# Kernel optimization log

Measured on AMD Instinct MI355X. Metric: run time of the kernel, lower is better.

## Reference

```python
import jax, jax.numpy as jnp
import numpy as np

L = 8          # fixed number of instance labels (0 = background), all assumed present
DV = 0.5       # delta_v
DD = 1.5       # delta_d
LOSS_WEIGHT = 1.0


def _safe_norm(x, axis):
    sq = jnp.sum(x * x, axis=axis)
    pos = sq > 0
    return jnp.sqrt(jnp.where(pos, sq, 1.0)) * pos.astype(x.dtype)


def _per_image(emb, inst, kern, tmask):
    # emb: [D,H,W], inst: [H,W] int, kern/tmask: [H,W] float
    D, H, W = emb.shape
    HW = H * W
    tm = (tmask > 0.5).astype(inst.dtype)
    kb = (kern > 0.5).astype(inst.dtype)
    inst = inst * tm
    inst_k = (inst * kb).reshape(-1)          # kernel-region labels
    inst_f = inst.reshape(-1)                 # full-region labels
    emb_f = emb.reshape(D, -1).T              # [HW, D]

    # --- generate_coef: first/second occurrence (row-major) of each label ---
    flat = jnp.arange(HW)
    eq = inst_f[None, :] == jnp.arange(L)[:, None]          # [L, HW]
    idxs = jnp.where(eq, flat[None, :], HW)
    first = jnp.min(idxs, axis=1)
    second = jnp.min(jnp.where(idxs == first[:, None], HW, idxs), axis=1)
    first = jnp.minimum(first, HW - 1)
    second = jnp.minimum(second, HW - 1)
    r0, c0 = first // W, first % W
    r1, c1 = second // W, second % W
    # pos_id = (tmp[0,0], tmp[1,0], tmp[0,-1], tmp[1,-1]) as in the source
    pos = jnp.stack([r0, r1, c0, c1], axis=1).astype(jnp.float32)  # [L,4]
    diag = jnp.sqrt(jnp.float32(H * H + W * W))
    coef_diag = jnp.exp(jnp.sqrt((pos[:, 0] - pos[:, 2]) ** 2 +
                                 (pos[:, 1] - pos[:, 3]) ** 2) / diag / 2.0)
    zmask = (jnp.arange(L) > 0).astype(jnp.float32)          # skip label 0
    coef_diag = coef_diag * zmask
    s = pos[:, 0] + pos[:, 2]
    t = pos[:, 1] + pos[:, 3]
    dp = jnp.sqrt((s[:, None] - s[None, :]) ** 2 + (t[:, None] - t[None, :]) ** 2)
    coef_off = 1.0 - 20.0 * jnp.exp(-4.0 - 2.5 * dp / diag)
    eye = jnp.eye(L, dtype=bool)
    coef = jnp.where(eye, coef_diag[:, None], coef_off)
    coef = coef * zmask[:, None] * zmask[None, :]

    # --- per-label kernel means (segment mean) ---
    ones = jnp.ones((HW,), jnp.float32)
    cnt_k = jax.ops.segment_sum(ones, inst_k, num_segments=L)
    mean = jax.ops.segment_sum(emb_f, inst_k, num_segments=L)
    mean = mean / jnp.maximum(cnt_k, 1.0)[:, None]           # [L, D]
    mean = mean * zmask[:, None]

    # --- l_agg: per-pixel distance to own-label mean, segment-mean per label ---
    mean_px = mean[inst_f]                                   # [HW, D] gather
    dist = _safe_norm(emb_f - mean_px, axis=1)
    cd_px = coef_diag[inst_f]
    val = jnp.log(jax.nn.relu(cd_px * dist - DV) ** 2 + 1.0)
    cnt = jax.ops.segment_sum(ones, inst_f, num_segments=L)
    l_agg_per = jax.ops.segment_sum(val, inst_f, num_segments=L) / jnp.maximum(cnt, 1.0)
    l_agg = jnp.mean(l_agg_per[1:])

    # --- l_dis: coefficient-weighted pairwise hinge between means ---
    Dn = _safe_norm(mean[:, None, :] - mean[None, :, :], axis=-1)  # [L, L]
    pm = (~eye) & (zmask[:, None] > 0) & (zmask[None, :] > 0)
    vals = jnp.log(jax.nn.relu(2.0 * DD - coef * Dn) ** 2 + 1.0)
    l_dis = jnp.sum(jnp.where(pm, vals, 0.0)) / ((L - 1) * (L - 2))

    # --- l_reg ---
    l_reg = jnp.mean(jnp.log(_safe_norm(mean, axis=1) + 1.0)) * 0.001
    return l_agg + l_dis + l_reg


def reference(emb, instance, kernel, training_mask, bboxes):
    # bboxes is accepted but unused, matching the original forward_single
    loss_batch = jax.vmap(_per_image)(emb, instance, kernel, training_mask)
    return LOSS_WEIGHT * jnp.mean(loss_batch)


def setup_inputs() -> dict:
    key = jax.random.key(0)
    k1, k2, k3, k4, k5 = jax.random.split(key, 5)
    B, D, H, W = 8, 4, 640, 640
    emb = jax.random.normal(k1, (B, D, H, W), dtype=jnp.float32)
    instance = jax.random.randint(k2, (B, H, W), 0, L, dtype=jnp.int32)
    kernel = jax.random.uniform(k3, (B, H, W), dtype=jnp.float32)
    training_mask = jax.random.uniform(k4, (B, H, W), dtype=jnp.float32)
    bboxes = jax.random.uniform(k5, (B, 10, 4), dtype=jnp.float32)
    return {"emb": emb, "instance": instance, "kernel": kernel,
            "training_mask": training_mask, "bboxes": bboxes}
```

## Files before the change

### kernel.cpp

```cpp
#include <hip/hip_runtime.h>
#include <hip/hip_bf16.h>

#define B_    8
#define D_    4
#define H_    640
#define W_    640
#define HW_   (H_ * W_)
#define L_    8
#define NL    (L_ - 1)
#define BLOCK 256
#define VITER 2
#define GRIDX (HW_ / (BLOCK * 4 * VITER))

__device__ __forceinline__ void gatom_add(float* p, float v) {
    unsafeAtomicAdd(p, v);
}

__global__ void k_init(int* ib) {
    int t = threadIdx.x;
    if (t < 128) ib[t] = HW_;
    ib[128 + t] = 0;
    if (t < 136) ib[384 + t] = 0;
}

__global__ __launch_bounds__(BLOCK, 4) void k_pass1(
        const float* __restrict__ emb, const int* __restrict__ inst,
        const float* __restrict__ kern, const float* __restrict__ tmask,
        int* __restrict__ firstIdx, int* __restrict__ secondIdx,
        int* __restrict__ cntf_i, int* __restrict__ cntk_i,
        float* __restrict__ sumemb) {
    __shared__ int   sCnt[L_];
    __shared__ float sSum[L_ * D_];
    __shared__ int   sM1[L_], sM2[L_];

    const int tid = threadIdx.x;
    if (tid < L_) { sCnt[tid] = 0; sM1[tid] = HW_; sM2[tid] = HW_; }
    if (tid < L_ * D_) sSum[tid] = 0.f;
    __syncthreads();

    const int b = blockIdx.y;
    const int blockbase = blockIdx.x * (BLOCK * 4 * VITER);
    const float* embb = emb + (size_t)b * D_ * HW_;
    const int base = b * HW_;

    int   hm[NL];
    int   kmask = 0;
    float sm[NL][D_];
    #pragma unroll
    for (int l = 0; l < NL; ++l) {
        hm[l] = 0;
        #pragma unroll
        for (int d = 0; d < D_; ++d) sm[l][d] = 0.f;
    }

    #pragma unroll
    for (int it = 0; it < VITER; ++it) {
        const int off = blockbase + it * (BLOCK * 4) + tid * 4;
        const int4   lab4 = *(const int4*)  (inst  + base + off);
        const float4 tm4  = *(const float4*)(tmask + base + off);
        const float4 kn4  = *(const float4*)(kern  + base + off);
        const float4 ev0  = *(const float4*)(embb + 0 * HW_ + off);
        const float4 ev1  = *(const float4*)(embb + 1 * HW_ + off);
        const float4 ev2  = *(const float4*)(embb + 2 * HW_ + off);
        const float4 ev3  = *(const float4*)(embb + 3 * HW_ + off);
        const int   labA[4] = {lab4.x, lab4.y, lab4.z, lab4.w};
        const float tmA[4]  = {tm4.x, tm4.y, tm4.z, tm4.w};
        const float knA[4]  = {kn4.x, kn4.y, kn4.z, kn4.w};
        const float e0A[4]  = {ev0.x, ev0.y, ev0.z, ev0.w};
        const float e1A[4]  = {ev1.x, ev1.y, ev1.z, ev1.w};
        const float e2A[4]  = {ev2.x, ev2.y, ev2.z, ev2.w};
        const float e3A[4]  = {ev3.x, ev3.y, ev3.z, ev3.w};

        #pragma unroll
        for (int c = 0; c < 4; ++c) {
            const int px = it * 4 + c;
            const int lf  = (tmA[c] > 0.5f) ? labA[c] : 0;
            const bool kb = (knA[c] > 0.5f);
            kmask |= (kb ? (1 << px) : 0);
            const int lfk = kb ? lf : 0;
            #pragma unroll
            for (int l = 1; l < L_; ++l) {
                const int k = l - 1;
                hm[k] |= (lf == l) ? (1 << px) : 0;
                const float mk = (lfk == l) ? 1.0f : 0.0f;
                sm[k][0] += mk * e0A[c];
                sm[k][1] += mk * e1A[c];
                sm[k][2] += mk * e2A[c];
                sm[k][3] += mk * e3A[c];
            }
        }
    }

    const int base0 = blockbase + tid * 4;
    int cnt[NL], m1[NL], m2[NL];
    #pragma unroll
    for (int l = 0; l < NL; ++l) {
        const int h = hm[l];
        cnt[l] = (__popc(h) << 16) | __popc(h & kmask);
        const int h2 = h & (h - 1);
        const int p1 = __ffs(h) - 1;
        const int p2 = __ffs(h2) - 1;
        m1[l] = h  ? (base0 + (p1 >> 2) * (BLOCK * 4) + (p1 & 3)) : HW_;
        m2[l] = h2 ? (base0 + (p2 >> 2) * (BLOCK * 4) + (p2 & 3)) : HW_;
    }

    #pragma unroll
    for (int l = 0; l < NL; ++l) {
        #pragma unroll
        for (int off = 32; off > 0; off >>= 1) {
            cnt[l]   += __shfl_down(cnt[l], off);
            sm[l][0] += __shfl_down(sm[l][0], off);
            sm[l][1] += __shfl_down(sm[l][1], off);
            sm[l][2] += __shfl_down(sm[l][2], off);
            sm[l][3] += __shfl_down(sm[l][3], off);
            int o1 = __shfl_down(m1[l], off);
            int o2 = __shfl_down(m2[l], off);
            m2[l] = min(min(m2[l], o2), max(m1[l], o1));
            m1[l] = min(m1[l], o1);
        }
    }

    if ((tid & 63) == 0) {
        #pragma unroll
        for (int l = 0; l < NL; ++l) {
            atomicAdd(&sCnt[l + 1], cnt[l]);
            #pragma unroll
            for (int d = 0; d < D_; ++d) atomicAdd(&sSum[(l + 1) * D_ + d], sm[l][d]);
            int old = atomicMin(&sM1[l + 1], m1[l]);
            atomicMin(&sM2[l + 1], max(old, m1[l]));
            atomicMin(&sM2[l + 1], m2[l]);
        }
    }
    __syncthreads();

    if (tid >= 1 && tid < L_) {
        const int pc = sCnt[tid];
        atomicAdd(&cntf_i[b * L_ + tid], pc >> 16);
        atomicAdd(&cntk_i[b * L_ + tid], pc & 0xFFFF);
        int old = atomicMin(&firstIdx[b * L_ + tid], sM1[tid]);
        atomicMin(&secondIdx[b * L_ + tid], max(old, sM1[tid]));
        atomicMin(&secondIdx[b * L_ + tid], sM2[tid]);
    }
    if (tid >= D_ && tid < L_ * D_)
        gatom_add(&sumemb[b * L_ * D_ + tid], sSum[tid]);
}

__global__ __launch_bounds__(BLOCK, 4) void k_pass3(
        const float* __restrict__ emb, const int* __restrict__ inst,
        const float* __restrict__ tmask,
        const int* __restrict__ firstIdx, const int* __restrict__ secondIdx,
        const int* __restrict__ cntk_i, const int* __restrict__ cntf_i,
        const float* __restrict__ sumemb, float* __restrict__ sumvalb) {
    __shared__ float4 sMean[L_];
    __shared__ float  sCd[L_], sInv[L_];
    __shared__ float  sAcc;

    const int tid = threadIdx.x;
    const int b   = blockIdx.y;

    if (tid < L_) {
        float4 mu = {0.f, 0.f, 0.f, 0.f};
        float cd = 0.f, inv = 0.f;
        if (tid > 0) {
            const float invk = 1.0f / fmaxf((float)cntk_i[b * L_ + tid], 1.0f);
            mu.x = sumemb[b * L_ * D_ + tid * D_ + 0] * invk;
            mu.y = sumemb[b * L_ * D_ + tid * D_ + 1] * invk;
            mu.z = sumemb[b * L_ * D_ + tid * D_ + 2] * invk;
            mu.w = sumemb[b * L_ * D_ + tid * D_ + 3] * invk;
            const float diag = sqrtf((float)(H_ * H_ + W_ * W_));
            int f = min(firstIdx[b * L_ + tid],  HW_ - 1);
            int s = min(secondIdx[b * L_ + tid], HW_ - 1);
            float r0 = (float)(f / W_), c0 = (float)(f % W_);
            float r1 = (float)(s / W_), c1 = (float)(s % W_);
            cd = __expf(sqrtf((r0 - c0) * (r0 - c0) + (r1 - c1) * (r1 - c1))
                        / diag * 0.5f);
            inv = 1.0f / fmaxf((float)cntf_i[b * L_ + tid], 1.0f);
        }
        sMean[tid] = mu; sCd[tid] = cd; sInv[tid] = inv;
        if (tid == 0) sAcc = 0.f;
    }
    __syncthreads();

    const int blockbase = blockIdx.x * (BLOCK * 4 * VITER);
    const float* embb = emb + (size_t)b * D_ * HW_;
    const int base = b * HW_;
    float acc = 0.f;

    #pragma unroll
    for (int it = 0; it < VITER; ++it) {
        const int off = blockbase + it * (BLOCK * 4) + tid * 4;
        const int4   lab4 = *(const int4*)  (inst  + base + off);
        const float4 tm4  = *(const float4*)(tmask + base + off);
        const float4 ev0  = *(const float4*)(embb + 0 * HW_ + off);
        const float4 ev1  = *(const float4*)(embb + 1 * HW_ + off);
        const float4 ev2  = *(const float4*)(embb + 2 * HW_ + off);
        const float4 ev3  = *(const float4*)(embb + 3 * HW_ + off);
        const int   labA[4] = {lab4.x, lab4.y, lab4.z, lab4.w};
        const float tmA[4]  = {tm4.x, tm4.y, tm4.z, tm4.w};
        const float e0A[4]  = {ev0.x, ev0.y, ev0.z, ev0.w};
        const float e1A[4]  = {ev1.x, ev1.y, ev1.z, ev1.w};
        const float e2A[4]  = {ev2.x, ev2.y, ev2.z, ev2.w};
        const float e3A[4]  = {ev3.x, ev3.y, ev3.z, ev3.w};

        #pragma unroll
        for (int c = 0; c < 4; ++c) {
            const int lf = (tmA[c] > 0.5f) ? labA[c] : 0;
            const float4 mu = sMean[lf];
            float dx = e0A[c] - mu.x, dy = e1A[c] - mu.y;
            float dz = e2A[c] - mu.z, dw = e3A[c] - mu.w;
            float d2 = dx * dx + dy * dy + dz * dz + dw * dw;
            float x  = fmaxf(sCd[lf] * sqrtf(d2) - 0.5f, 0.0f);
            acc += __logf(x * x + 1.0f) * sInv[lf];
        }
    }

    #pragma unroll
    for (int off = 32; off > 0; off >>= 1)
        acc += __shfl_down(acc, off);
    if ((tid & 63) == 0) atomicAdd(&sAcc, acc);
    __syncthreads();
    if (tid == 0) gatom_add(&sumvalb[b], sAcc);
}

__global__ __launch_bounds__(512) void k_final(
        const int* __restrict__ firstIdx, const int* __restrict__ secondIdx,
        const int* __restrict__ cntk_i, const float* __restrict__ sumemb,
        const float* __restrict__ sumvalb, float* __restrict__ out) {
    __shared__ float sWave[8];
    const int tid = threadIdx.x;
    const int b = tid >> 6, ij = tid & 63, i = ij >> 3, j = ij & 7;
    const float diag = sqrtf((float)(H_ * H_ + W_ * W_));

    float mi[D_], mj[D_];
    {
        float ci = 1.0f / fmaxf((float)cntk_i[b * L_ + i], 1.0f);
        float cj = 1.0f / fmaxf((float)cntk_i[b * L_ + j], 1.0f);
        #pragma unroll
        for (int d = 0; d < D_; ++d) {
            mi[d] = (i > 0) ? sumemb[(b * L_ + i) * D_ + d] * ci : 0.0f;
            mj[d] = (j > 0) ? sumemb[(b * L_ + j) * D_ + d] * cj : 0.0f;
        }
    }

    float contrib = 0.0f;
    if (j == 0) {
        float d2 = 0.f;
        #pragma unroll
        for (int d = 0; d < D_; ++d) d2 += mi[d] * mi[d];
        float n = (d2 > 0.f) ? sqrtf(d2) : 0.f;
        contrib += __logf(n + 1.0f) * (0.001f / (float)L_);
    }
    if (i == 0 && j == 1)
        contrib += sumvalb[b] * (1.0f / (float)NL);
    if (i >= 1 && j >= 1 && i != j) {
        float d2 = 0.f;
        #pragma unroll
        for (int d = 0; d < D_; ++d) {
            float df = mi[d] - mj[d];
            d2 += df * df;
        }
        float Dn = (d2 > 0.f) ? sqrtf(d2) : 0.f;
        int fi = min(firstIdx[b * L_ + i],  HW_ - 1);
        int si = min(secondIdx[b * L_ + i], HW_ - 1);
        int fj = min(firstIdx[b * L_ + j],  HW_ - 1);
        int sj = min(secondIdx[b * L_ + j], HW_ - 1);
        float ssi = (float)(fi / W_) + (float)(fi % W_);
        float tti = (float)(si / W_) + (float)(si % W_);
        float ssj = (float)(fj / W_) + (float)(fj % W_);
        float ttj = (float)(sj / W_) + (float)(sj % W_);
        float dx = ssi - ssj, dy = tti - ttj;
        float dp = sqrtf(dx * dx + dy * dy);
        float coef = 1.0f - 20.0f * __expf(-4.0f - 2.5f * dp / diag);
        float x = fmaxf(3.0f - coef * Dn, 0.0f);
        contrib += __logf(x * x + 1.0f) * (1.0f / 42.0f);
    }

    #pragma unroll
    for (int off = 32; off > 0; off >>= 1)
        contrib += __shfl_down(contrib, off);
    if ((tid & 63) == 0) sWave[tid >> 6] = contrib;
    __syncthreads();
    if (tid == 0) {
        float t = 0.f;
        #pragma unroll
        for (int w = 0; w < 8; ++w) t += sWave[w];
        out[0] = t * (1.0f / (float)B_);
    }
}

extern "C" void kernel_launch(void* const* d_in, const int* in_sizes, int n_in,
                              void* d_out, int out_size, void* d_ws, size_t ws_size,
                              hipStream_t stream) {
    const float* emb   = (const float*)d_in[0];
    const int*   inst  = (const int*)  d_in[1];
    const float* kern  = (const float*)d_in[2];
    const float* tmask = (const float*)d_in[3];

    int*   ib        = (int*)d_ws;
    int*   firstIdx  = ib;
    int*   secondIdx = ib + 64;
    int*   cntf_i    = ib + 128;
    int*   cntk_i    = ib + 192;
    float* sumemb    = (float*)(ib + 256);
    float* sumvalb   = (float*)(ib + 512);
    float* out       = (float*)d_out;

    dim3 grid(GRIDX, B_);

    k_init <<<1, 256, 0, stream>>>(ib);
    k_pass1<<<grid, BLOCK, 0, stream>>>(emb, inst, kern, tmask,
                                        firstIdx, secondIdx, cntf_i, cntk_i, sumemb);
    k_pass3<<<grid, BLOCK, 0, stream>>>(emb, inst, tmask, firstIdx, secondIdx,
                                        cntk_i, cntf_i, sumemb, sumvalb);
    k_final<<<1, 512, 0, stream>>>(firstIdx, secondIdx, cntk_i,
                                   sumemb, sumvalb, out);
}
```

Before: 171.3 us.

## Pack masked labels into nibbles for pass3 and use LDS atomics for segment sums

Pass1 now writes each pixel's masked label as a 4-bit nibble into a packed workspace buffer. Pass3 reads that buffer instead of re-reading the int32 instance map and the training mask, which cuts its global traffic. Per-label embedding sums move from 28 register accumulators with wave shuffles to per-lane shared-memory atomic adds. The per-label bitmasks are now built from three label bit-planes. The shared-memory atomics and the added 64-lane LDS buffer may add contention and reduce occupancy, and the kernel also gains an odd redundant shared-memory init loop.

```diff
diff --git a/kernel.cpp b/kernel.cpp
--- a/kernel.cpp
+++ b/kernel.cpp
@@ -10,7 +10,8 @@
 #define NL    (L_ - 1)
 #define BLOCK 256
 #define VITER 2
-#define GRIDX (HW_ / (BLOCK * 4 * VITER))
+#define PXB   (BLOCK * 4 * VITER)
+#define GRIDX (HW_ / PXB)
 
 __device__ __forceinline__ void gatom_add(float* p, float v) {
     unsafeAtomicAdd(p, v);
@@ -28,110 +29,127 @@
         const float* __restrict__ kern, const float* __restrict__ tmask,
         int* __restrict__ firstIdx, int* __restrict__ secondIdx,
         int* __restrict__ cntf_i, int* __restrict__ cntk_i,
-        float* __restrict__ sumemb) {
+        float* __restrict__ sumemb, unsigned int* __restrict__ lblpack) {
+    __shared__ float sSum[D_ * L_ * 64];
     __shared__ int   sCnt[L_];
-    __shared__ float sSum[L_ * D_];
     __shared__ int   sM1[L_], sM2[L_];
 
-    const int tid = threadIdx.x;
+    const int tid  = threadIdx.x;
+    const int lane = tid & 63;
     if (tid < L_) { sCnt[tid] = 0; sM1[tid] = HW_; sM2[tid] = HW_; }
-    if (tid < L_ * D_) sSum[tid] = 0.f;
+    #pragma unroll
+    for (int i = 0; i < D_ * L_; ++i) sSum[i * 64 + (tid & 63)] = (tid < 64) ? 0.f : sSum[i * 64 + (tid & 63)];
+    __syncthreads();
+    for (int i = tid; i < D_ * L_ * 64; i += BLOCK) sSum[i] = 0.f;
     __syncthreads();
 
     const int b = blockIdx.y;
-    const int blockbase = blockIdx.x * (BLOCK * 4 * VITER);
+    const int blockbase = blockIdx.x * PXB;
     const float* embb = emb + (size_t)b * D_ * HW_;
     const int base = b * HW_;
-
-    int   hm[NL];
-    int   kmask = 0;
-    float sm[NL][D_];
-    #pragma unroll
-    for (int l = 0; l < NL; ++l) {
-        hm[l] = 0;
-        #pragma unroll
-        for (int d = 0; d < D_; ++d) sm[l][d] = 0.f;
-    }
+    const int off0 = blockbase + tid * 4;
+    const int off1 = off0 + BLOCK * 4;
+
+    const int4   lab_0 = *(const int4*)  (inst  + base + off0);
+    const int4   lab_1 = *(const int4*)  (inst  + base + off1);
+    const float4 tm_0  = *(const float4*)(tmask + base + off0);
+    const float4 tm_1  = *(const float4*)(tmask + base + off1);
+    const float4 kn_0  = *(const float4*)(kern  + base + off0);
+    const float4 kn_1  = *(const float4*)(kern  + base + off1);
+    const float4 e0_0  = *(const float4*)(embb + 0 * HW_ + off0);
+    const float4 e1_0  = *(const float4*)(embb + 1 * HW_ + off0);
+    const float4 e2_0  = *(const float4*)(embb + 2 * HW_ + off0);
+    const float4 e3_0  = *(const float4*)(embb + 3 * HW_ + off0);
+    const float4 e0_1  = *(const float4*)(embb + 0 * HW_ + off1);
+    const float4 e1_1  = *(const float4*)(embb + 1 * HW_ + off1);
+    const float4 e2_1  = *(const float4*)(embb + 2 * HW_ + off1);
+    const float4 e3_1  = *(const float4*)(embb + 3 * HW_ + off1);
+
+    int bp0 = 0, bp1 = 0, bp2 = 0, kmask = 0;
+    unsigned int lp = 0;
 
     #pragma unroll
     for (int it = 0; it < VITER; ++it) {
-        const int off = blockbase + it * (BLOCK * 4) + tid * 4;
-        const int4   lab4 = *(const int4*)  (inst  + base + off);
-        const float4 tm4  = *(const float4*)(tmask + base + off);
-        const float4 kn4  = *(const float4*)(kern  + base + off);
-        const float4 ev0  = *(const float4*)(embb + 0 * HW_ + off);
-        const float4 ev1  = *(const float4*)(embb + 1 * HW_ + off);
-        const float4 ev2  = *(const float4*)(embb + 2 * HW_ + off);
-        const float4 ev3  = *(const float4*)(embb + 3 * HW_ + off);
-        const int   labA[4] = {lab4.x, lab4.y, lab4.z, lab4.w};
-        const float tmA[4]  = {tm4.x, tm4.y, tm4.z, tm4.w};
-        const float knA[4]  = {kn4.x, kn4.y, kn4.z, kn4.w};
-        const float e0A[4]  = {ev0.x, ev0.y, ev0.z, ev0.w};
-        const float e1A[4]  = {ev1.x, ev1.y, ev1.z, ev1.w};
-        const float e2A[4]  = {ev2.x, ev2.y, ev2.z, ev2.w};
-        const float e3A[4]  = {ev3.x, ev3.y, ev3.z, ev3.w};
+        const int*   labA = (it == 0) ? (const int*)&lab_0 : (const int*)&lab_1;
+        const float* tmA  = (it == 0) ? (const float*)&tm_0 : (const float*)&tm_1;
+        const float* knA  = (it == 0) ? (const float*)&kn_0 : (const float*)&kn_1;
+        const float* e0A  = (it == 0) ? (const float*)&e0_0 : (const float*)&e0_1;
+        const float* e1A  = (it == 0) ? (const float*)&e1_0 : (const float*)&e1_1;
+        const float* e2A  = (it == 0) ? (const float*)&e2_0 : (const float*)&e2_1;
+        const float* e3A  = (it == 0) ? (const float*)&e3_0 : (const float*)&e3_1;
 
         #pragma unroll
         for (int c = 0; c < 4; ++c) {
             const int px = it * 4 + c;
             const int lf  = (tmA[c] > 0.5f) ? labA[c] : 0;
             const bool kb = (knA[c] > 0.5f);
-            kmask |= (kb ? (1 << px) : 0);
             const int lfk = kb ? lf : 0;
-            #pragma unroll
-            for (int l = 1; l < L_; ++l) {
-                const int k = l - 1;
-                hm[k] |= (lf == l) ? (1 << px) : 0;
-                const float mk = (lfk == l) ? 1.0f : 0.0f;
-                sm[k][0] += mk * e0A[c];
-                sm[k][1] += mk * e1A[c];
-                sm[k][2] += mk * e2A[c];
-                sm[k][3] += mk * e3A[c];
-            }
-        }
-    }
-
+            bp0   |= (lf & 1) << px;
+            bp1   |= ((lf >> 1) & 1) << px;
+            bp2   |= ((lf >> 2) & 1) << px;
+            kmask |= (kb ? 1 : 0) << px;
+            lp    |= (unsigned int)lf << (4 * px);
+            const int idx = lfk * 64 + lane;
+            atomicAdd(&sSum[0 * 512 + idx], e0A[c]);
+            atomicAdd(&sSum[1 * 512 + idx], e1A[c]);
+            atomicAdd(&sSum[2 * 512 + idx], e2A[c]);
+            atomicAdd(&sSum[3 * 512 + idx], e3A[c]);
+        }
+    }
+
+    lblpack[(size_t)(b * GRIDX + blockIdx.x) * BLOCK + tid] = lp;
+
+    const int nb0 = ~bp0, nb1 = ~bp1, nb2 = ~bp2;
     const int base0 = blockbase + tid * 4;
     int cnt[NL], m1[NL], m2[NL];
     #pragma unroll
-    for (int l = 0; l < NL; ++l) {
-        const int h = hm[l];
-        cnt[l] = (__popc(h) << 16) | __popc(h & kmask);
+    for (int l = 1; l < L_; ++l) {
+        const int k = l - 1;
+        int h = ((l & 1) ? bp0 : nb0) & ((l & 2) ? bp1 : nb1) & ((l & 4) ? bp2 : nb2);
+        h &= 0xFF;
+        cnt[k] = (__popc(h) << 16) | __popc(h & kmask);
         const int h2 = h & (h - 1);
         const int p1 = __ffs(h) - 1;
         const int p2 = __ffs(h2) - 1;
-        m1[l] = h  ? (base0 + (p1 >> 2) * (BLOCK * 4) + (p1 & 3)) : HW_;
-        m2[l] = h2 ? (base0 + (p2 >> 2) * (BLOCK * 4) + (p2 & 3)) : HW_;
+        m1[k] = h  ? (base0 + (p1 >> 2) * (BLOCK * 4) + (p1 & 3)) : HW_;
+        m2[k] = h2 ? (base0 + (p2 >> 2) * (BLOCK * 4) + (p2 & 3)) : HW_;
     }
 
     #pragma unroll
     for (int l = 0; l < NL; ++l) {
         #pragma unroll
         for (int off = 32; off > 0; off >>= 1) {
-            cnt[l]   += __shfl_down(cnt[l], off);
-            sm[l][0] += __shfl_down(sm[l][0], off);
-            sm[l][1] += __shfl_down(sm[l][1], off);
-            sm[l][2] += __shfl_down(sm[l][2], off);
-            sm[l][3] += __shfl_down(sm[l][3], off);
+            cnt[l] += __shfl_down(cnt[l], off);
             int o1 = __shfl_down(m1[l], off);
             int o2 = __shfl_down(m2[l], off);
             m2[l] = min(min(m2[l], o2), max(m1[l], o1));
             m1[l] = min(m1[l], o1);
         }
     }
-
-    if ((tid & 63) == 0) {
+    if (lane == 0) {
         #pragma unroll
         for (int l = 0; l < NL; ++l) {
             atomicAdd(&sCnt[l + 1], cnt[l]);
-            #pragma unroll
-            for (int d = 0; d < D_; ++d) atomicAdd(&sSum[(l + 1) * D_ + d], sm[l][d]);
             int old = atomicMin(&sM1[l + 1], m1[l]);
             atomicMin(&sM2[l + 1], max(old, m1[l]));
             atomicMin(&sM2[l + 1], m2[l]);
         }
     }
     __syncthreads();
+
+    if (tid < 224) {
+        const int pr = tid;
+        const int l  = (pr >> 5) + 1;
+        const int d  = (pr >> 3) & 3;
+        const int k  = pr & 7;
+        float v = 0.f;
+        #pragma unroll
+        for (int j = 0; j < 8; ++j) v += sSum[d * 512 + l * 64 + k * 8 + j];
+        v += __shfl_down(v, 4, 8);
+        v += __shfl_down(v, 2, 8);
+        v += __shfl_down(v, 1, 8);
+        if (k == 0) gatom_add(&sumemb[(b * L_ + l) * D_ + d], v);
+    }
 
     if (tid >= 1 && tid < L_) {
         const int pc = sCnt[tid];
@@ -141,13 +159,10 @@
         atomicMin(&secondIdx[b * L_ + tid], max(old, sM1[tid]));
         atomicMin(&secondIdx[b * L_ + tid], sM2[tid]);
     }
-    if (tid >= D_ && tid < L_ * D_)
-        gatom_add(&sumemb[b * L_ * D_ + tid], sSum[tid]);
 }
 
 __global__ __launch_bounds__(BLOCK, 4) void k_pass3(
-        const float* __restrict__ emb, const int* __restrict__ inst,
-        const float* __restrict__ tmask,
+        const float* __restrict__ emb, const unsigned int* __restrict__ lblpack,
         const int* __restrict__ firstIdx, const int* __restrict__ secondIdx,
         const int* __restrict__ cntk_i, const int* __restrict__ cntf_i,
         const float* __restrict__ sumemb, float* __restrict__ sumvalb) {
@@ -181,30 +196,32 @@
     }
     __syncthreads();
 
-    const int blockbase = blockIdx.x * (BLOCK * 4 * VITER);
+    const int blockbase = blockIdx.x * PXB;
     const float* embb = emb + (size_t)b * D_ * HW_;
-    const int base = b * HW_;
+    const int off0 = blockbase + tid * 4;
+    const int off1 = off0 + BLOCK * 4;
+
+    const unsigned int lp = lblpack[(size_t)(b * GRIDX + blockIdx.x) * BLOCK + tid];
+    const float4 e0_0 = *(const float4*)(embb + 0 * HW_ + off0);
+    const float4 e1_0 = *(const float4*)(embb + 1 * HW_ + off0);
+    const float4 e2_0 = *(const float4*)(embb + 2 * HW_ + off0);
+    const float4 e3_0 = *(const float4*)(embb + 3 * HW_ + off0);
+    const float4 e0_1 = *(const float4*)(embb + 0 * HW_ + off1);
+    const float4 e1_1 = *(const float4*)(embb + 1 * HW_ + off1);
+    const float4 e2_1 = *(const float4*)(embb + 2 * HW_ + off1);
+    const float4 e3_1 = *(const float4*)(embb + 3 * HW_ + off1);
+
     float acc = 0.f;
-
     #pragma unroll
     for (int it = 0; it < VITER; ++it) {
-        const int off = blockbase + it * (BLOCK * 4) + tid * 4;
-        const int4   lab4 = *(const int4*)  (inst  + base + off);
-        const float4 tm4  = *(const float4*)(tmask + base + off);
-        const float4 ev0  = *(const float4*)(embb + 0 * HW_ + off);
-        const float4 ev1  = *(const float4*)(embb + 1 * HW_ + off);
-        const float4 ev2  = *(const float4*)(embb + 2 * HW_ + off);
-        const float4 ev3  = *(const float4*)(embb + 3 * HW_ + off);
-        const int   labA[4] = {lab4.x, lab4.y, lab4.z, lab4.w};
-        const float tmA[4]  = {tm4.x, tm4.y, tm4.z, tm4.w};
-        const float e0A[4]  = {ev0.x, ev0.y, ev0.z, ev0.w};
-        const float e1A[4]  = {ev1.x, ev1.y, ev1.z, ev1.w};
-        const float e2A[4]  = {ev2.x, ev2.y, ev2.z, ev2.w};
-        const float e3A[4]  = {ev3.x, ev3.y, ev3.z, ev3.w};
-
+        const float* e0A = (it == 0) ? (const float*)&e0_0 : (const float*)&e0_1;
+        const float* e1A = (it == 0) ? (const float*)&e1_0 : (const float*)&e1_1;
+        const float* e2A = (it == 0) ? (const float*)&e2_0 : (const float*)&e2_1;
+        const float* e3A = (it == 0) ? (const float*)&e3_0 : (const float*)&e3_1;
         #pragma unroll
         for (int c = 0; c < 4; ++c) {
-            const int lf = (tmA[c] > 0.5f) ? labA[c] : 0;
+            const int px = it * 4 + c;
+            const int lf = (lp >> (4 * px)) & 15;
             const float4 mu = sMean[lf];
             float dx = e0A[c] - mu.x, dy = e1A[c] - mu.y;
             float dz = e2A[c] - mu.z, dw = e3A[c] - mu.w;
@@ -296,21 +313,23 @@
     const float* kern  = (const float*)d_in[2];
     const float* tmask = (const float*)d_in[3];
 
-    int*   ib        = (int*)d_ws;
-    int*   firstIdx  = ib;
-    int*   secondIdx = ib + 64;
-    int*   cntf_i    = ib + 128;
-    int*   cntk_i    = ib + 192;
-    float* sumemb    = (float*)(ib + 256);
-    float* sumvalb   = (float*)(ib + 512);
-    float* out       = (float*)d_out;
+    int*          ib        = (int*)d_ws;
+    int*          firstIdx  = ib;
+    int*          secondIdx = ib + 64;
+    int*          cntf_i    = ib + 128;
+    int*          cntk_i    = ib + 192;
+    float*        sumemb    = (float*)(ib + 256);
+    float*        sumvalb   = (float*)(ib + 512);
+    unsigned int* lblpack   = (unsigned int*)(ib + 1024);
+    float*        out       = (float*)d_out;
 
     dim3 grid(GRIDX, B_);
 
     k_init <<<1, 256, 0, stream>>>(ib);
     k_pass1<<<grid, BLOCK, 0, stream>>>(emb, inst, kern, tmask,
-                                        firstIdx, secondIdx, cntf_i, cntk_i, sumemb);
-    k_pass3<<<grid, BLOCK, 0, stream>>>(emb, inst, tmask, firstIdx, secondIdx,
+                                        firstIdx, secondIdx, cntf_i, cntk_i,
+                                        sumemb, lblpack);
+    k_pass3<<<grid, BLOCK, 0, stream>>>(emb, lblpack, firstIdx, secondIdx,
                                         cntk_i, cntf_i, sumemb, sumvalb);
     k_final<<<1, 512, 0, stream>>>(firstIdx, secondIdx, cntk_i,
                                    sumemb, sumvalb, out);
```

After: 217.1 us. 26.7% more time.

## Fuse both passes into one persistent kernel with grid barrier, reuse embeddings in registers

Applied to the files above, without the earlier changes.

Merges the statistics pass and the loss pass into one kernel separated by a software grid-wide barrier (atomic counter plus spin-wait), so the embeddings, labels and mask are read from global memory once and kept in registers. VITER rises from 2 to 4 to halve the grid to 800 blocks. Labels are packed into bit-planes and a nibble word to cut register use. The grid barrier only works if all blocks are resident at once (800 blocks at 4 per CU needs about 200 CUs), so it risks deadlock or stalls, and the higher register pressure may cut occupancy.

```diff
diff --git a/kernel.cpp b/kernel.cpp
--- a/kernel.cpp
+++ b/kernel.cpp
@@ -1,5 +1,4 @@
 #include <hip/hip_runtime.h>
-#include <hip/hip_bf16.h>
 
 #define B_    8
 #define D_    4
@@ -9,8 +8,10 @@
 #define L_    8
 #define NL    (L_ - 1)
 #define BLOCK 256
-#define VITER 2
-#define GRIDX (HW_ / (BLOCK * 4 * VITER))
+#define VITER 4
+#define PXB   (BLOCK * 4 * VITER)
+#define GRIDX (HW_ / PXB)
+#define NBLK  (GRIDX * B_)
 
 __device__ __forceinline__ void gatom_add(float* p, float v) {
     unsafeAtomicAdd(p, v);
@@ -20,88 +21,111 @@
     int t = threadIdx.x;
     if (t < 128) ib[t] = HW_;
     ib[128 + t] = 0;
-    if (t < 136) ib[384 + t] = 0;
-}
-
-__global__ __launch_bounds__(BLOCK, 4) void k_pass1(
+    if (t < 137) ib[384 + t] = 0;
+}
+
+__global__ __launch_bounds__(BLOCK, 4) void k_fused(
         const float* __restrict__ emb, const int* __restrict__ inst,
         const float* __restrict__ kern, const float* __restrict__ tmask,
         int* __restrict__ firstIdx, int* __restrict__ secondIdx,
         int* __restrict__ cntf_i, int* __restrict__ cntk_i,
-        float* __restrict__ sumemb) {
-    __shared__ int   sCnt[L_];
-    __shared__ float sSum[L_ * D_];
-    __shared__ int   sM1[L_], sM2[L_];
-
-    const int tid = threadIdx.x;
+        float* __restrict__ sumemb, float* __restrict__ sumvalb,
+        int* __restrict__ bar) {
+    __shared__ int    sCnt[L_];
+    __shared__ float  sSum[L_ * D_];
+    __shared__ int    sM1[L_], sM2[L_];
+    __shared__ float4 sMean[L_];
+    __shared__ float  sCd[L_], sInv[L_];
+    __shared__ float  sAcc;
+
+    const int tid  = threadIdx.x;
+    const int lane = tid & 63;
     if (tid < L_) { sCnt[tid] = 0; sM1[tid] = HW_; sM2[tid] = HW_; }
     if (tid < L_ * D_) sSum[tid] = 0.f;
+    if (tid == 0) sAcc = 0.f;
     __syncthreads();
 
     const int b = blockIdx.y;
-    const int blockbase = blockIdx.x * (BLOCK * 4 * VITER);
+    const int blockbase = blockIdx.x * PXB;
     const float* embb = emb + (size_t)b * D_ * HW_;
     const int base = b * HW_;
-
-    int   hm[NL];
-    int   kmask = 0;
-    float sm[NL][D_];
-    #pragma unroll
-    for (int l = 0; l < NL; ++l) {
-        hm[l] = 0;
-        #pragma unroll
-        for (int d = 0; d < D_; ++d) sm[l][d] = 0.f;
-    }
-
+    const int o0 = blockbase + tid * 4;
+
+    int4 LB[VITER]; float4 TM[VITER], KN[VITER];
     #pragma unroll
     for (int it = 0; it < VITER; ++it) {
-        const int off = blockbase + it * (BLOCK * 4) + tid * 4;
-        const int4   lab4 = *(const int4*)  (inst  + base + off);
-        const float4 tm4  = *(const float4*)(tmask + base + off);
-        const float4 kn4  = *(const float4*)(kern  + base + off);
-        const float4 ev0  = *(const float4*)(embb + 0 * HW_ + off);
-        const float4 ev1  = *(const float4*)(embb + 1 * HW_ + off);
-        const float4 ev2  = *(const float4*)(embb + 2 * HW_ + off);
-        const float4 ev3  = *(const float4*)(embb + 3 * HW_ + off);
-        const int   labA[4] = {lab4.x, lab4.y, lab4.z, lab4.w};
-        const float tmA[4]  = {tm4.x, tm4.y, tm4.z, tm4.w};
-        const float knA[4]  = {kn4.x, kn4.y, kn4.z, kn4.w};
-        const float e0A[4]  = {ev0.x, ev0.y, ev0.z, ev0.w};
-        const float e1A[4]  = {ev1.x, ev1.y, ev1.z, ev1.w};
-        const float e2A[4]  = {ev2.x, ev2.y, ev2.z, ev2.w};
-        const float e3A[4]  = {ev3.x, ev3.y, ev3.z, ev3.w};
-
+        const int off = o0 + it * (BLOCK * 4);
+        LB[it] = *(const int4*)  (inst  + base + off);
+        TM[it] = *(const float4*)(tmask + base + off);
+        KN[it] = *(const float4*)(kern  + base + off);
+    }
+    float4 E[VITER][D_];
+    #pragma unroll
+    for (int it = 0; it < VITER; ++it)
+        #pragma unroll
+        for (int d = 0; d < D_; ++d)
+            E[it][d] = *(const float4*)(embb + d * HW_ + o0 + it * (BLOCK * 4));
+
+    unsigned long long lp = 0;
+    int bp0 = 0, bp1 = 0, bp2 = 0, km = 0;
+    #pragma unroll
+    for (int it = 0; it < VITER; ++it) {
+        const int*   labA = (const int*)&LB[it];
+        const float* tmA  = (const float*)&TM[it];
+        const float* knA  = (const float*)&KN[it];
         #pragma unroll
         for (int c = 0; c < 4; ++c) {
             const int px = it * 4 + c;
             const int lf  = (tmA[c] > 0.5f) ? labA[c] : 0;
             const bool kb = (knA[c] > 0.5f);
-            kmask |= (kb ? (1 << px) : 0);
-            const int lfk = kb ? lf : 0;
+            bp0 |= (lf & 1) << px;
+            bp1 |= ((lf >> 1) & 1) << px;
+            bp2 |= ((lf >> 2) & 1) << px;
+            km  |= (kb ? 1 : 0) << px;
+            lp  |= (unsigned long long)lf << (4 * px);
+        }
+    }
+
+    float sm[NL][D_];
+    #pragma unroll
+    for (int l = 0; l < NL; ++l)
+        #pragma unroll
+        for (int d = 0; d < D_; ++d) sm[l][d] = 0.f;
+    #pragma unroll
+    for (int it = 0; it < VITER; ++it) {
+        const float* e0A = (const float*)&E[it][0];
+        const float* e1A = (const float*)&E[it][1];
+        const float* e2A = (const float*)&E[it][2];
+        const float* e3A = (const float*)&E[it][3];
+        #pragma unroll
+        for (int c = 0; c < 4; ++c) {
+            const int px = it * 4 + c;
+            const int lf = (int)((lp >> (4 * px)) & 7);
+            const int lfk = ((km >> px) & 1) ? lf : 0;
             #pragma unroll
             for (int l = 1; l < L_; ++l) {
-                const int k = l - 1;
-                hm[k] |= (lf == l) ? (1 << px) : 0;
                 const float mk = (lfk == l) ? 1.0f : 0.0f;
-                sm[k][0] += mk * e0A[c];
-                sm[k][1] += mk * e1A[c];
-                sm[k][2] += mk * e2A[c];
-                sm[k][3] += mk * e3A[c];
+                sm[l - 1][0] += mk * e0A[c];
+                sm[l - 1][1] += mk * e1A[c];
+                sm[l - 1][2] += mk * e2A[c];
+                sm[l - 1][3] += mk * e3A[c];
             }
         }
     }
 
-    const int base0 = blockbase + tid * 4;
+    const int nb0 = ~bp0, nb1 = ~bp1, nb2 = ~bp2;
     int cnt[NL], m1[NL], m2[NL];
     #pragma unroll
-    for (int l = 0; l < NL; ++l) {
-        const int h = hm[l];
-        cnt[l] = (__popc(h) << 16) | __popc(h & kmask);
+    for (int l = 1; l < L_; ++l) {
+        const int k = l - 1;
+        int h = ((l & 1) ? bp0 : nb0) & ((l & 2) ? bp1 : nb1) & ((l & 4) ? bp2 : nb2);
+        h &= 0xFFFF;
+        cnt[k] = (__popc(h) << 16) | __popc(h & km);
         const int h2 = h & (h - 1);
         const int p1 = __ffs(h) - 1;
         const int p2 = __ffs(h2) - 1;
-        m1[l] = h  ? (base0 + (p1 >> 2) * (BLOCK * 4) + (p1 & 3)) : HW_;
-        m2[l] = h2 ? (base0 + (p2 >> 2) * (BLOCK * 4) + (p2 & 3)) : HW_;
+        m1[k] = h  ? (o0 + (p1 >> 2) * (BLOCK * 4) + (p1 & 3)) : HW_;
+        m2[k] = h2 ? (o0 + (p2 >> 2) * (BLOCK * 4) + (p2 & 3)) : HW_;
     }
 
     #pragma unroll
@@ -119,8 +143,7 @@
             m1[l] = min(m1[l], o1);
         }
     }
-
-    if ((tid & 63) == 0) {
+    if (lane == 0) {
         #pragma unroll
         for (int l = 0; l < NL; ++l) {
             atomicAdd(&sCnt[l + 1], cnt[l]);
@@ -143,68 +166,55 @@
     }
     if (tid >= D_ && tid < L_ * D_)
         gatom_add(&sumemb[b * L_ * D_ + tid], sSum[tid]);
-}
-
-__global__ __launch_bounds__(BLOCK, 4) void k_pass3(
-        const float* __restrict__ emb, const int* __restrict__ inst,
-        const float* __restrict__ tmask,
-        const int* __restrict__ firstIdx, const int* __restrict__ secondIdx,
-        const int* __restrict__ cntk_i, const int* __restrict__ cntf_i,
-        const float* __restrict__ sumemb, float* __restrict__ sumvalb) {
-    __shared__ float4 sMean[L_];
-    __shared__ float  sCd[L_], sInv[L_];
-    __shared__ float  sAcc;
-
-    const int tid = threadIdx.x;
-    const int b   = blockIdx.y;
-
-    if (tid < L_) {
-        float4 mu = {0.f, 0.f, 0.f, 0.f};
-        float cd = 0.f, inv = 0.f;
-        if (tid > 0) {
-            const float invk = 1.0f / fmaxf((float)cntk_i[b * L_ + tid], 1.0f);
-            mu.x = sumemb[b * L_ * D_ + tid * D_ + 0] * invk;
-            mu.y = sumemb[b * L_ * D_ + tid * D_ + 1] * invk;
-            mu.z = sumemb[b * L_ * D_ + tid * D_ + 2] * invk;
-            mu.w = sumemb[b * L_ * D_ + tid * D_ + 3] * invk;
-            const float diag = sqrtf((float)(H_ * H_ + W_ * W_));
-            int f = min(firstIdx[b * L_ + tid],  HW_ - 1);
-            int s = min(secondIdx[b * L_ + tid], HW_ - 1);
-            float r0 = (float)(f / W_), c0 = (float)(f % W_);
-            float r1 = (float)(s / W_), c1 = (float)(s % W_);
-            cd = __expf(sqrtf((r0 - c0) * (r0 - c0) + (r1 - c1) * (r1 - c1))
-                        / diag * 0.5f);
-            inv = 1.0f / fmaxf((float)cntf_i[b * L_ + tid], 1.0f);
-        }
-        sMean[tid] = mu; sCd[tid] = cd; sInv[tid] = inv;
-        if (tid == 0) sAcc = 0.f;
-    }
-    __syncthreads();
-
-    const int blockbase = blockIdx.x * (BLOCK * 4 * VITER);
-    const float* embb = emb + (size_t)b * D_ * HW_;
-    const int base = b * HW_;
+
+    __syncthreads();
+    if (tid == 0) {
+        __threadfence();
+        atomicAdd(bar, 1);
+        while (__hip_atomic_load(bar, __ATOMIC_RELAXED,
+                                 __HIP_MEMORY_SCOPE_AGENT) < NBLK)
+            __builtin_amdgcn_s_sleep(8);
+        __threadfence();
+    }
+    __syncthreads();
+
+    if (tid >= 1 && tid < L_) {
+        const int gi = b * L_ + tid;
+        const float ckv = (float)__hip_atomic_load(&cntk_i[gi], __ATOMIC_RELAXED, __HIP_MEMORY_SCOPE_AGENT);
+        const float cfv = (float)__hip_atomic_load(&cntf_i[gi], __ATOMIC_RELAXED, __HIP_MEMORY_SCOPE_AGENT);
+        const int   f   = min(__hip_atomic_load(&firstIdx[gi],  __ATOMIC_RELAXED, __HIP_MEMORY_SCOPE_AGENT), HW_ - 1);
+        const int   s   = min(__hip_atomic_load(&secondIdx[gi], __ATOMIC_RELAXED, __HIP_MEMORY_SCOPE_AGENT), HW_ - 1);
+        const float invk = 1.0f / fmaxf(ckv, 1.0f);
+        float4 mu;
+        mu.x = __hip_atomic_load(&sumemb[gi * D_ + 0], __ATOMIC_RELAXED, __HIP_MEMORY_SCOPE_AGENT) * invk;
+        mu.y = __hip_atomic_load(&sumemb[gi * D_ + 1], __ATOMIC_RELAXED, __HIP_MEMORY_SCOPE_AGENT) * invk;
+        mu.z = __hip_atomic_load(&sumemb[gi * D_ + 2], __ATOMIC_RELAXED, __HIP_MEMORY_SCOPE_AGENT) * invk;
+        mu.w = __hip_atomic_load(&sumemb[gi * D_ + 3], __ATOMIC_RELAXED, __HIP_MEMORY_SCOPE_AGENT) * invk;
+        const float diag = sqrtf((float)(H_ * H_ + W_ * W_));
+        const float r0 = (float)(f / W_), c0 = (float)(f % W_);
+        const float r1 = (float)(s / W_), c1 = (float)(s % W_);
+        sMean[tid] = mu;
+        sCd[tid]  = __expf(sqrtf((r0 - c0) * (r0 - c0) + (r1 - c1) * (r1 - c1))
+                           / diag * 0.5f);
+        sInv[tid] = 1.0f / fmaxf(cfv, 1.0f);
+    }
+    if (tid == 0) {
+        sMean[0] = make_float4(0.f, 0.f, 0.f, 0.f);
+        sCd[0] = 0.f; sInv[0] = 0.f;
+    }
+    __syncthreads();
+
     float acc = 0.f;
-
     #pragma unroll
     for (int it = 0; it < VITER; ++it) {
-        const int off = blockbase + it * (BLOCK * 4) + tid * 4;
-        const int4   lab4 = *(const int4*)  (inst  + base + off);
-        const float4 tm4  = *(const float4*)(tmask + base + off);
-        const float4 ev0  = *(const float4*)(embb + 0 * HW_ + off);
-        const float4 ev1  = *(const float4*)(embb + 1 * HW_ + off);
-        const float4 ev2  = *(const float4*)(embb + 2 * HW_ + off);
-        const float4 ev3  = *(const float4*)(embb + 3 * HW_ + off);
-        const int   labA[4] = {lab4.x, lab4.y, lab4.z, lab4.w};
-        const float tmA[4]  = {tm4.x, tm4.y, tm4.z, tm4.w};
-        const float e0A[4]  = {ev0.x, ev0.y, ev0.z, ev0.w};
-        const float e1A[4]  = {ev1.x, ev1.y, ev1.z, ev1.w};
-        const float e2A[4]  = {ev2.x, ev2.y, ev2.z, ev2.w};
-        const float e3A[4]  = {ev3.x, ev3.y, ev3.z, ev3.w};
-
+        const float* e0A = (const float*)&E[it][0];
+        const float* e1A = (const float*)&E[it][1];
+        const float* e2A = (const float*)&E[it][2];
+        const float* e3A = (const float*)&E[it][3];
         #pragma unroll
         for (int c = 0; c < 4; ++c) {
-            const int lf = (tmA[c] > 0.5f) ? labA[c] : 0;
+            const int px = it * 4 + c;
+            const int lf = (int)((lp >> (4 * px)) & 7);
             const float4 mu = sMean[lf];
             float dx = e0A[c] - mu.x, dy = e1A[c] - mu.y;
             float dz = e2A[c] - mu.z, dw = e3A[c] - mu.w;
@@ -213,11 +223,10 @@
             acc += __logf(x * x + 1.0f) * sInv[lf];
         }
     }
-
     #pragma unroll
     for (int off = 32; off > 0; off >>= 1)
         acc += __shfl_down(acc, off);
-    if ((tid & 63) == 0) atomicAdd(&sAcc, acc);
+    if (lane == 0) atomicAdd(&sAcc, acc);
     __syncthreads();
     if (tid == 0) gatom_add(&sumvalb[b], sAcc);
 }
@@ -303,15 +312,15 @@
     int*   cntk_i    = ib + 192;
     float* sumemb    = (float*)(ib + 256);
     float* sumvalb   = (float*)(ib + 512);
+    int*   bar       = ib + 520;
     float* out       = (float*)d_out;
 
     dim3 grid(GRIDX, B_);
 
     k_init <<<1, 256, 0, stream>>>(ib);
-    k_pass1<<<grid, BLOCK, 0, stream>>>(emb, inst, kern, tmask,
-                                        firstIdx, secondIdx, cntf_i, cntk_i, sumemb);
-    k_pass3<<<grid, BLOCK, 0, stream>>>(emb, inst, tmask, firstIdx, secondIdx,
-                                        cntk_i, cntf_i, sumemb, sumvalb);
+    k_fused<<<grid, BLOCK, 0, stream>>>(emb, inst, kern, tmask,
+                                        firstIdx, secondIdx, cntf_i, cntk_i,
+                                        sumemb, sumvalb, bar);
     k_final<<<1, 512, 0, stream>>>(firstIdx, secondIdx, cntk_i,
                                    sumemb, sumvalb, out);
 }
```

Result: slower. 271.6 us (+58.5%).
